# Optimization experiments

Hardware: AMD Instinct MI355X
Metric: run time of the kernel (lower is better)

## Reference

```python
import jax, jax.numpy as jnp
import numpy as np

B, N, DIM = 2, 512, 512
HEADS, DIM_HEAD, MAX_LEN = 8, 64, 1024


def _skew(QEr):
    # pad last dim on the left by 1, reshape (n, n+1) -> (n+1, n), drop first row
    padded = jnp.pad(QEr, ((0, 0), (0, 0), (0, 0), (1, 0)))
    b, h, r, c = padded.shape
    return padded.reshape(b, h, c, r)[:, :, 1:, :]


def _fft_multiply_parallel(A, x):
    # A: [b,h,n,n] decay matrix; x: [b,h,n,d]
    b, h, n, d = x.shape
    # y = [last column of A, first row of A] -> [b,h,2n]
    y = jnp.concatenate([A[:, :, :, -1], A[:, :, 0, :]], axis=-1)
    v = jnp.concatenate([x, jnp.zeros_like(x)], axis=-2)  # zero-pad rows n -> 2n
    # Faithful to the original torch code: fftn over ALL axes (incl. batch/head),
    # then ifft over the LAST axis only, then slice back to n rows.
    H = jnp.fft.fftn(y)[:, :, :, None] * jnp.fft.fftn(v)
    return jnp.fft.ifft(H)[:, :, :n, :]


def _forward(x, Wq, Wk, Wv, Er):
    b, n, _ = x.shape

    def split_heads(t):
        return t.reshape(b, n, HEADS, DIM_HEAD).transpose(0, 2, 1, 3)  # [b,h,n,d]

    q = split_heads(x @ Wq)
    k = split_heads(x @ Wk)
    v = split_heads(x @ Wv)
    # global (Frobenius) norm over the full tensor, as torch.norm(t)
    q = q / jnp.linalg.norm(q)
    k = k / jnp.linalg.norm(k)
    q_ = jax.nn.elu(q)
    k_ = jax.nn.elu(k)

    Er_t = Er[MAX_LEN - n:, :].T        # [d, n]
    QEr = q @ Er_t                       # [b,h,n,n]
    c = jnp.exp(_skew(QEr))              # relative-position decay, [b,h,n,n]

    a_1 = jnp.einsum('bhnx,bhny->bhnxy', k_, v).reshape(b, HEADS, n, DIM_HEAD * DIM_HEAD)
    d_2 = _fft_multiply_parallel(c, k_)                                   # [b,h,n,d] complex
    d_1 = _fft_multiply_parallel(c, a_1).reshape(b, HEADS, n, DIM_HEAD, DIM_HEAD)

    top = jnp.einsum('bhnx,bhnyz->bhnz', q_, d_1)    # complex [b,h,n,d]
    bottom = jnp.einsum('bhnx,bhny->bhny', q_, d_2)  # complex [b,h,n,d]
    return top / bottom


def setup_inputs() -> dict:
    key = jax.random.key(0)
    k1, k2, k3, k4, k5 = jax.random.split(key, 5)
    s = jnp.float32(1.0 / np.sqrt(DIM))
    return {
        'x': jax.random.normal(k1, (B, N, DIM), dtype=jnp.float32),
        'Wq': jax.random.normal(k2, (DIM, HEADS * DIM_HEAD), dtype=jnp.float32) * s,
        'Wk': jax.random.normal(k3, (DIM, HEADS * DIM_HEAD), dtype=jnp.float32) * s,
        'Wv': jax.random.normal(k4, (DIM, HEADS * DIM_HEAD), dtype=jnp.float32) * s,
        'Er': jax.random.normal(k5, (MAX_LEN, DIM_HEAD), dtype=jnp.float32),
    }


def reference(x, Wq, Wk, Wv, Er):
    return _forward(x, Wq, Wk, Wv, Er)
```

## Files before the change

### kernel.cpp

```cpp
#include <hip/hip_runtime.h>
#include <math.h>


#define DIMX 512
#define NPOS 512
#define PADIDX(m) ((m) + ((m) >> 4))

typedef unsigned short ushort_t;
typedef unsigned int uint_t;
typedef __bf16 bf16x8 __attribute__((ext_vector_type(8)));
typedef float floatx4 __attribute__((ext_vector_type(4)));

static __device__ inline ushort_t f2bf(float f) {
    uint_t u = __float_as_uint(f);
    u = u + 0x7FFFu + ((u >> 16) & 1u);
    return (ushort_t)(u >> 16);
}
static __device__ inline float bf2f(ushort_t h) {
    return __uint_as_float(((uint_t)h) << 16);
}

#define BFLY(lo, hi, tw) do {                                   \
    const float sr_ = (lo).x - (hi).x, si_ = (lo).y - (hi).y;   \
    (lo).x += (hi).x; (lo).y += (hi).y;                         \
    (hi).x = sr_ * (tw).x - si_ * (tw).y;                       \
    (hi).y = sr_ * (tw).y + si_ * (tw).x;                       \
} while (0)

__global__ __launch_bounds__(256)
void conv_kernel(const float* __restrict__ x,
                 const float* __restrict__ Wk, const float* __restrict__ Wv,
                 ushort_t* __restrict__ xh, ushort_t* __restrict__ xl,
                 ushort_t* __restrict__ wth, ushort_t* __restrict__ wtl,
                 float2* __restrict__ twd)
{
    const int blk = blockIdx.x;
    const int t = threadIdx.x;
    if (blk < 512) {
        const int idx4 = blk * 256 + t;
        const float4 v = ((const float4*)x)[idx4];
        const float vf[4] = {v.x, v.y, v.z, v.w};
        ushort_t h[4], l[4];
        #pragma unroll
        for (int e = 0; e < 4; ++e) {
            h[e] = f2bf(vf[e]);
            l[e] = f2bf(vf[e] - bf2f(h[e]));
        }
        const ushort4 hv4 = make_ushort4(h[0], h[1], h[2], h[3]);
        const ushort4 lv4 = make_ushort4(l[0], l[1], l[2], l[3]);
        *(ushort4*)(xh + (size_t)idx4 * 4) = hv4;
        *(ushort4*)(xl + (size_t)idx4 * 4) = lv4;
    } else if (blk < 1024) {
        __shared__ float tile[32][33];
        const int b2 = blk - 512;
        const int s  = b2 >> 8;
        const int kt = (b2 >> 4) & 15;
        const int nt = b2 & 15;
        const int c  = t & 31, r4 = t >> 5;
        const float* __restrict__ W = s ? Wv : Wk;
        #pragma unroll
        for (int i = 0; i < 4; ++i) {
            const int row = r4 + i * 8;
            tile[row][c] = W[(size_t)(kt * 32 + row) * 512 + nt * 32 + c];
        }
        __syncthreads();
        #pragma unroll
        for (int i = 0; i < 4; ++i) {
            const int nl = r4 + i * 8;
            const float v = tile[c][nl];
            const ushort_t h = f2bf(v);
            const ushort_t l = f2bf(v - bf2f(h));
            const size_t o = (size_t)(s * 512 + nt * 32 + nl) * 512 + kt * 32 + c;
            wth[o] = h;
            wtl[o] = l;
        }
    } else {
        const int jj = (blk - 1024) * 256 + t;
        double s, cc;
        sincos(-6.2831853071795864769 * (double)jj / 1024.0, &s, &cc);
        twd[jj] = make_float2((float)cc, (float)s);
    }
}

__global__ __launch_bounds__(256)
void gemm_mfma_kernel(const ushort_t* __restrict__ xh, const ushort_t* __restrict__ xl,
                      const ushort_t* __restrict__ wth, const ushort_t* __restrict__ wtl,
                      float* __restrict__ K, float* __restrict__ V,
                      float* __restrict__ partials)
{
    const int blk = blockIdx.x;
    const int ct = blk >> 5;
    const int rt = blk & 31;
    const int t = threadIdx.x;
    const int w = t >> 6, lane = t & 63;
    const int qd = lane >> 4, lm = lane & 15;

    const int mrow = rt * 32 + (w & 1) * 16 + lm;
    const int wcol = (w >> 1) * 32;
    const size_t aoff = (size_t)mrow * 512 + qd * 8;

    __shared__ __align__(16) ushort_t Bs[2][2][8][64][8];
    __shared__ float red[4];

    #define STAGE(buf_, k0_)                                                     \
    {                                                                            \
        _Pragma("unroll")                                                        \
        for (int i = 0; i < 4; ++i) {                                            \
            const int seg = w * 4 + i;                                           \
            const int arr_ = seg >> 3, kq_ = seg & 7;                            \
            const ushort_t* src_ = (arr_ ? wtl : wth)                            \
                + (size_t)(ct * 64 + lane) * 512 + (k0_) + kq_ * 8;              \
            __builtin_amdgcn_global_load_lds(                                    \
                (const __attribute__((address_space(1))) uint_t*)src_,           \
                (__attribute__((address_space(3))) uint_t*)&Bs[buf_][arr_][kq_][0][0], \
                16, 0, 0);                                                       \
        }                                                                        \
    }

    floatx4 acc0 = {0.f, 0.f, 0.f, 0.f};
    floatx4 acc1 = {0.f, 0.f, 0.f, 0.f};

    STAGE(0, 0)
    for (int ks = 0; ks < 8; ++ks) {
        __syncthreads();
        const int buf = ks & 1;
        const int k0 = ks * 64;
        if (ks < 7) STAGE(buf ^ 1, k0 + 64)
        #pragma unroll
        for (int s2 = 0; s2 < 2; ++s2) {
            const bf16x8 Ah = *(const bf16x8*)&xh[aoff + k0 + s2 * 32];
            const bf16x8 Al = *(const bf16x8*)&xl[aoff + k0 + s2 * 32];
            const int kq = s2 * 4 + qd;
            const bf16x8 B0h = *(const bf16x8*)Bs[buf][0][kq][wcol + lm];
            const bf16x8 B0l = *(const bf16x8*)Bs[buf][1][kq][wcol + lm];
            const bf16x8 B1h = *(const bf16x8*)Bs[buf][0][kq][wcol + 16 + lm];
            const bf16x8 B1l = *(const bf16x8*)Bs[buf][1][kq][wcol + 16 + lm];
            acc0 = __builtin_amdgcn_mfma_f32_16x16x32_bf16(Ah, B0h, acc0, 0, 0, 0);
            acc0 = __builtin_amdgcn_mfma_f32_16x16x32_bf16(Ah, B0l, acc0, 0, 0, 0);
            acc0 = __builtin_amdgcn_mfma_f32_16x16x32_bf16(Al, B0h, acc0, 0, 0, 0);
            acc1 = __builtin_amdgcn_mfma_f32_16x16x32_bf16(Ah, B1h, acc1, 0, 0, 0);
            acc1 = __builtin_amdgcn_mfma_f32_16x16x32_bf16(Ah, B1l, acc1, 0, 0, 0);
            acc1 = __builtin_amdgcn_mfma_f32_16x16x32_bf16(Al, B1h, acc1, 0, 0, 0);
        }
    }
    #undef STAGE

    float ss = 0.f;
    const int orow0 = rt * 32 + (w & 1) * 16 + qd * 4;
    float* __restrict__ O = (ct < 8) ? K : V;
    const int cb = (ct < 8) ? 0 : 512;
    const int c0 = ct * 64 + wcol + lm - cb;
    #pragma unroll
    for (int r = 0; r < 4; ++r) {
        const size_t row = orow0 + r;
        const float v0 = acc0[r], v1 = acc1[r];
        O[row * 512 + c0]      = v0;
        O[row * 512 + c0 + 16] = v1;
        if (ct < 8) ss += v0 * v0 + v1 * v1;
    }
    #pragma unroll
    for (int off = 32; off > 0; off >>= 1)
        ss += __shfl_down(ss, off, 64);
    if (lane == 0) red[w] = ss;
    __syncthreads();
    if (t == 0) partials[blk] = red[0] + red[1] + red[2] + red[3];
}

__device__ __constant__ float C8[8] = {
    1.f, 0.70710678118654752440f, 0.f, -0.70710678118654752440f,
   -1.f, -0.70710678118654752440f, 0.f, 0.70710678118654752440f };
__device__ __constant__ float S8[8] = {
    0.f, -0.70710678118654752440f, -1.f, -0.70710678118654752440f,
    0.f,  0.70710678118654752440f,  1.f,  0.70710678118654752440f };

__global__ __launch_bounds__(256)
void stage1_kernel(const float* __restrict__ K,
                   const float* __restrict__ V,
                   const float* __restrict__ partials,
                   float2* __restrict__ Gk,
                   float2* __restrict__ Gp)
{
    const int m = blockIdx.x;
    const int t = threadIdx.x;
    __shared__ float kk[2][8][64];
    __shared__ float pp[2][8][64];
    __shared__ float skp[16][4];
    __shared__ float sk[2][8];
    __shared__ float sred[4];

    float p = partials[t] + partials[t + 256];
    #pragma unroll
    for (int off = 32; off > 0; off >>= 1)
        p += __shfl_down(p, off, 64);
    if ((t & 63) == 0) sred[t >> 6] = p;
    __syncthreads();
    const float scale = (float)(1.0 / sqrt((double)sred[0] + (double)sred[1] +
                                           (double)sred[2] + (double)sred[3]));

    {
        const int e0 = t * 4;
        const int b = e0 >> 9, rem = e0 & 511, h = rem >> 6, z = rem & 63;
        const size_t src = (size_t)(b * 512 + m) * DIMX + h * 64 + z;
        const float4 kv4 = *(const float4*)&K[src];
        const float4 vv4 = *(const float4*)&V[src];
        const float kf[4] = {kv4.x, kv4.y, kv4.z, kv4.w};
        const float vf[4] = {vv4.x, vv4.y, vv4.z, vv4.w};
        #pragma unroll
        for (int e = 0; e < 4; ++e) {
            const float kv = kf[e] * scale;
            kk[b][h][z + e] = kv > 0.f ? kv : expm1f(kv);
            pp[b][h][z + e] = vf[e];
        }
    }
    __syncthreads();
    if (t < 64) {
        const int bh = t >> 2, q = t & 3;
        float s = 0.f;
        #pragma unroll
        for (int zz = 0; zz < 16; ++zz) s += kk[bh >> 3][bh & 7][q * 16 + zz];
        skp[bh][q] = s;
    }
    __syncthreads();
    if (t < 16) sk[t >> 3][t & 7] = skp[t][0] + skp[t][1] + skp[t][2] + skp[t][3];
    __syncthreads();

    for (int e2 = t; e2 < 512; e2 += 256) {
        const int be = e2 >> 5;
        const int zp = e2 & 31;
        const int beta = be >> 3, eta = be & 7;
        float kr[2] = {0.f, 0.f}, ki[2] = {0.f, 0.f};
        float pr[2] = {0.f, 0.f}, pim[2] = {0.f, 0.f};
        #pragma unroll
        for (int b = 0; b < 2; ++b) {
            const float sgn = (beta & b) ? -1.f : 1.f;
            #pragma unroll
            for (int h = 0; h < 8; ++h) {
                const int ph = (eta * h) & 7;
                const float cr = C8[ph], ci = S8[ph];
                const float skv = sk[b][h];
                #pragma unroll
                for (int zz = 0; zz < 2; ++zz) {
                    const int z = zp * 2 + zz;
                    const float a = kk[b][h][z] * sgn;
                    kr[zz] = fmaf(a, cr, kr[zz]);
                    ki[zz] = fmaf(a, ci, ki[zz]);
                    const float p2 = (pp[b][h][z] * skv) * sgn;
                    pr[zz]  = fmaf(p2, cr, pr[zz]);
                    pim[zz] = fmaf(p2, ci, pim[zz]);
                }
            }
        }
        const float4 rk = make_float4(kr[0], ki[0], kr[1], ki[1]);
        const float4 rp = make_float4(pr[0], pim[0], pr[1], pim[1]);
        const size_t o = ((size_t)be * NPOS + m) * 64 + zp * 2;
        *(float4*)&Gk[o] = rk;
        *(float4*)&Gp[o] = rp;
    }
}

__global__ __launch_bounds__(256)
void fft_div_kernel(const float2* __restrict__ Gk,
                    const float2* __restrict__ Gp,
                    const float2* __restrict__ twd,
                    float* __restrict__ out, int out_cplx)
{
    const int blk = blockIdx.x;
    const int j  = blk & 7;
    const int l  = (blk >> 3) & 3;
    const int be = blk >> 5;
    const int zg = j * 4 + l;
    const int t  = threadIdx.x;

    __shared__ float2 g[4][1088];
    __shared__ float2 w[544];

    for (int jj = t; jj < 512; jj += 256)
        w[PADIDX(jj)] = twd[jj];
    for (int e = t; e < 1024; e += 256) {
        const int a = e >> 9;
        const int m = e & 511;
        const float4 v4 = *(const float4*)&(a ? Gp : Gk)[((size_t)be * NPOS + m) * 64 + zg * 2];
        g[a * 2 + 0][PADIDX(m)] = make_float2(v4.x, v4.y);
        g[a * 2 + 1][PADIDX(m)] = make_float2(v4.z, v4.w);
    }
    __syncthreads();

    const int wv   = t >> 6;
    const int lane = t & 63;

    #pragma unroll
    for (int qh = 0; qh < 2; ++qh) {
        const int hh  = 1 - qh;
        const int arr = wv;
        const int jo  = lane;
        float2 f[8];
        #pragma unroll
        for (int k = 0; k < 8; ++k)
            f[k] = g[arr][PADIDX(jo + k * 64)];
        if (hh == 1) {
            #pragma unroll
            for (int k = 0; k < 8; ++k) {
                const float2 tw = w[PADIDX(jo + k * 64)];
                f[k] = make_float2(f[k].x * tw.x - f[k].y * tw.y,
                                   f[k].x * tw.y + f[k].y * tw.x);
            }
        }
        #pragma unroll
        for (int k = 0; k < 4; ++k) {
            const float2 tw = w[PADIDX(2 * jo + 128 * k)];
            BFLY(f[k], f[k + 4], tw);
        }
        {
            const float2 tw0 = w[PADIDX(4 * jo)];
            const float2 tw1 = w[PADIDX(4 * jo + 256)];
            BFLY(f[0], f[2], tw0); BFLY(f[1], f[3], tw1);
            BFLY(f[4], f[6], tw0); BFLY(f[5], f[7], tw1);
        }
        {
            const float2 tw = w[PADIDX(8 * jo)];
            BFLY(f[0], f[1], tw); BFLY(f[2], f[3], tw);
            BFLY(f[4], f[5], tw); BFLY(f[6], f[7], tw);
        }
        #pragma unroll
        for (int k = 0; k < 8; ++k)
            g[arr][PADIDX(hh * 512 + jo + k * 64)] = f[k];
    }

    #pragma unroll
    for (int q = 0; q < 2; ++q) {
        const int arr = wv;
        const int b64 = q * 8 + (lane >> 3);
        const int jo  = lane & 7;
        const int e0  = b64 * 64 + jo;
        float2 f[8];
        #pragma unroll
        for (int k = 0; k < 8; ++k)
            f[k] = g[arr][PADIDX(e0 + 8 * k)];
        #pragma unroll
        for (int k = 0; k < 4; ++k) {
            const float2 tw = w[PADIDX(16 * jo + 128 * k)];
            BFLY(f[k], f[k + 4], tw);
        }
        {
            const float2 tw0 = w[PADIDX(32 * jo)];
            const float2 tw1 = w[PADIDX(32 * jo + 256)];
            BFLY(f[0], f[2], tw0); BFLY(f[1], f[3], tw1);
            BFLY(f[4], f[6], tw0); BFLY(f[5], f[7], tw1);
        }
        {
            const float2 tw = w[PADIDX(64 * jo)];
            BFLY(f[0], f[1], tw); BFLY(f[2], f[3], tw);
            BFLY(f[4], f[5], tw); BFLY(f[6], f[7], tw);
        }
        #pragma unroll
        for (int k = 0; k < 8; ++k)
            g[arr][PADIDX(e0 + 8 * k)] = f[k];
    }

    #pragma unroll
    for (int q = 0; q < 2; ++q) {
        const int arr = wv;
        const int b8  = q * 64 + lane;
        const int e0  = b8 * 8;
        float2 f[8];
        #pragma unroll
        for (int k = 0; k < 8; ++k)
            f[k] = g[arr][PADIDX(e0 + k)];
        BFLY(f[0], f[4], w[PADIDX(0)]);
        BFLY(f[1], f[5], w[PADIDX(128)]);
        BFLY(f[2], f[6], w[PADIDX(256)]);
        BFLY(f[3], f[7], w[PADIDX(384)]);
        {
            const float2 tw0 = w[PADIDX(0)];
            const float2 tw1 = w[PADIDX(256)];
            BFLY(f[0], f[2], tw0); BFLY(f[1], f[3], tw1);
            BFLY(f[4], f[6], tw0); BFLY(f[5], f[7], tw1);
        }
        f[0].x += f[1].x; f[0].y += f[1].y;
        f[2].x += f[3].x; f[2].y += f[3].y;
        f[4].x += f[5].x; f[4].y += f[5].y;
        f[6].x += f[7].x; f[6].y += f[7].y;
        g[arr][PADIDX(e0 + 0)] = f[0];
        g[arr][PADIDX(e0 + 2)] = f[2];
        g[arr][PADIDX(e0 + 4)] = f[4];
        g[arr][PADIDX(e0 + 6)] = f[6];
    }
    __syncthreads();

    for (int e2 = t; e2 < 512; e2 += 256) {
        const int i  = e2;
        const int pi = PADIDX(2 * i);
        const int mu = (int)(__brev((unsigned)i) >> 23);
        float4 res;
        #pragma unroll
        for (int zi = 0; zi < 2; ++zi) {
            const float2 D  = g[zi][pi];
            const float2 Nm = g[2 + zi][pi];
            const float inv = 1.f / (D.x * D.x + D.y * D.y);
            const float rr = (Nm.x * D.x + Nm.y * D.y) * inv;
            const float ri = (Nm.y * D.x - Nm.x * D.y) * inv;
            if (zi == 0) { res.x = rr; res.y = ri; }
            else         { res.z = rr; res.w = ri; }
        }
        const size_t o = ((size_t)be * NPOS + mu) * 64 + zg * 2;
        if (out_cplx) {
            *(float4*)&((float2*)out)[o] = res;
        } else {
            out[o]     = res.x;
            out[o + 1] = res.z;
        }
    }
}

__global__ __launch_bounds__(256)
void gemm_kv_kernel(const float* __restrict__ x,
                    const float* __restrict__ Wk,
                    const float* __restrict__ Wv,
                    float* __restrict__ K,
                    float* __restrict__ V,
                    float* __restrict__ partials)
{
    const int blk  = blockIdx.x;
    const int sel  = (blk >> 2) & 1;
    const int cg2  = blk & 3;
    const int rt   = blk >> 3;
    const int row0 = rt * 16;
    const int col0 = cg2 * 128;
    const int t    = threadIdx.x;
    const int tc   = t & 31;
    const int tr   = t >> 5;
    const float* __restrict__ W   = sel ? Wv : Wk;
    float* __restrict__       Out = sel ? V  : K;

    __shared__ float xs[16][DIMX];
    __shared__ float red[4];

    #pragma unroll
    for (int jj = 0; jj < 8; ++jj) {
        const int f = t + jj * 256;
        const int row = f >> 7, c4 = f & 127;
        *(float4*)&xs[row][c4 * 4] = *(const float4*)&x[(size_t)(row0 + row) * DIMX + c4 * 4];
    }
    __syncthreads();

    const float* Wb = W + col0 + tc * 4;
    float4 wA[8], wB[8];
    #pragma unroll
    for (int jj = 0; jj < 8; ++jj) wA[jj] = *(const float4*)&Wb[(size_t)(jj) * DIMX];
    #pragma unroll
    for (int jj = 0; jj < 8; ++jj) wB[jj] = *(const float4*)&Wb[(size_t)(8 + jj) * DIMX];

    float acc[2][4] = {{0,0,0,0},{0,0,0,0}};
    const int r0 = tr * 2;

    #define COMPUTE_CHUNK(WREG, CH)                                            \
        {   float4 xv0a = *(const float4*)&xs[r0][(CH) * 8];                   \
            float4 xv0b = *(const float4*)&xs[r0][(CH) * 8 + 4];               \
            float4 xv1a = *(const float4*)&xs[r0 + 1][(CH) * 8];               \
            float4 xv1b = *(const float4*)&xs[r0 + 1][(CH) * 8 + 4];           \
            _Pragma("unroll")                                                  \
            for (int kk = 0; kk < 4; ++kk) {                                   \
                const float x0 = (&xv0a.x)[kk], x1 = (&xv1a.x)[kk];            \
                _Pragma("unroll")                                              \
                for (int cc = 0; cc < 4; ++cc) {                               \
                    acc[0][cc] = fmaf(x0, (&WREG[kk].x)[cc], acc[0][cc]);      \
                    acc[1][cc] = fmaf(x1, (&WREG[kk].x)[cc], acc[1][cc]);      \
                } }                                                            \
            _Pragma("unroll")                                                  \
            for (int kk = 0; kk < 4; ++kk) {                                   \
                const float x0 = (&xv0b.x)[kk], x1 = (&xv1b.x)[kk];            \
                _Pragma("unroll")                                              \
                for (int cc = 0; cc < 4; ++cc) {                               \
                    acc[0][cc] = fmaf(x0, (&WREG[kk + 4].x)[cc], acc[0][cc]);  \
                    acc[1][cc] = fmaf(x1, (&WREG[kk + 4].x)[cc], acc[1][cc]);  \
                } } }

    for (int ch = 0; ch < 64; ch += 2) {
        COMPUTE_CHUNK(wA, ch)
        if (ch < 62) {
            #pragma unroll
            for (int jj = 0; jj < 8; ++jj)
                wA[jj] = *(const float4*)&Wb[(size_t)((ch + 2) * 8 + jj) * DIMX];
        }
        COMPUTE_CHUNK(wB, ch + 1)
        if (ch < 62) {
            #pragma unroll
            for (int jj = 0; jj < 8; ++jj)
                wB[jj] = *(const float4*)&Wb[(size_t)((ch + 3) * 8 + jj) * DIMX];
        }
    }
    #undef COMPUTE_CHUNK

    float ss = 0.f;
    #pragma unroll
    for (int i = 0; i < 2; ++i) {
        const int row = row0 + r0 + i;
        const float4 o = make_float4(acc[i][0], acc[i][1], acc[i][2], acc[i][3]);
        *(float4*)&Out[(size_t)row * DIMX + col0 + tc * 4] = o;
        ss += o.x * o.x + o.y * o.y + o.z * o.z + o.w * o.w;
    }
    if (sel == 0) {
        #pragma unroll
        for (int off = 32; off > 0; off >>= 1)
            ss += __shfl_down(ss, off, 64);
        if ((t & 63) == 0) red[t >> 6] = ss;
        __syncthreads();
        if (t == 0) partials[blk] = red[0] + red[1] + red[2] + red[3];
    } else {
        if (t == 0) partials[blk] = 0.f;
    }
}

__global__ __launch_bounds__(256)
void mdft_fallback_kernel(const float2* __restrict__ Gk,
                          const float2* __restrict__ Gp,
                          float* __restrict__ out,
                          int out_cplx)
{
    const int blk = blockIdx.x;
    const int be = blk >> 6, z = blk & 63;
    const int t = threadIdx.x;
    __shared__ float2 gk[512];
    __shared__ float2 gp[512];
    __shared__ float2 w[1024];

    for (int m = t; m < 512; m += 256) {
        const size_t idx = ((size_t)be * NPOS + m) * 64 + z;
        gk[m] = Gk[idx];
        gp[m] = Gp[idx];
    }
    for (int jj = t; jj < 1024; jj += 256) {
        double s, c;
        sincos(-6.2831853071795864769 * (double)jj / 1024.0, &s, &c);
        w[jj] = make_float2((float)c, (float)s);
    }
    __syncthreads();

    #pragma unroll
    for (int half = 0; half < 2; ++half) {
        const int mu = t + half * 256;
        double dr = 0.0, di = 0.0, nr = 0.0, ni = 0.0;
        int idx = 0;
        for (int m = 0; m < 512; ++m) {
            const float2 tw = w[idx];
            idx = (idx + mu) & 1023;
            const float2 a = gk[m];
            dr += (double)(a.x * tw.x - a.y * tw.y);
            di += (double)(a.x * tw.y + a.y * tw.x);
            const float2 p2 = gp[m];
            nr += (double)(p2.x * tw.x - p2.y * tw.y);
            ni += (double)(p2.x * tw.y + p2.y * tw.x);
        }
        const double dmag = dr * dr + di * di;
        const double orr = (nr * dr + ni * di) / dmag;
        const double oii = (ni * dr - nr * di) / dmag;
        const size_t o = ((size_t)be * NPOS + mu) * 64 + z;
        if (out_cplx) {
            out[2 * o]     = (float)orr;
            out[2 * o + 1] = (float)oii;
        } else {
            out[o] = (float)orr;
        }
    }
}

extern "C" void kernel_launch(void* const* d_in, const int* in_sizes, int n_in,
                              void* d_out, int out_size, void* d_ws, size_t ws_size,
                              hipStream_t stream)
{
    const float* x  = (const float*)d_in[0];
    const float* Wk = (const float*)d_in[2];
    const float* Wv = (const float*)d_in[3];
    float* out = (float*)d_out;

    char* ws = (char*)d_ws;
    float*  K    = (float*)(ws);
    float*  V    = (float*)(ws + (size_t)2097152);
    float2* Gk   = (float2*)(ws + (size_t)4194304);
    float*  part = (float*)(ws + (size_t)8388608);
    const int out_cplx = (out_size >= 2 * 2 * 8 * 512 * 64) ? 1 : 0;

    const bool ws_big = (ws_size >= (size_t)20971520);
    float2* Gp = ws_big ? (float2*)(ws + (size_t)8390656)
                        : (float2*)d_out;

    if (ws_big) {
        ushort_t* xh  = (ushort_t*)(ws + (size_t)16777216);
        ushort_t* xl  = (ushort_t*)(ws + (size_t)17825792);
        ushort_t* wth = (ushort_t*)(ws + (size_t)18874368);
        ushort_t* wtl = (ushort_t*)(ws + (size_t)19922944);
        float2*   twd = (float2*)(ws + (size_t)12584960);
        hipLaunchKernelGGL(conv_kernel, dim3(1026), dim3(256), 0, stream,
                           x, Wk, Wv, xh, xl, wth, wtl, twd);
        hipLaunchKernelGGL(gemm_mfma_kernel, dim3(512), dim3(256), 0, stream,
                           xh, xl, wth, wtl, K, V, part);
        hipLaunchKernelGGL(stage1_kernel, dim3(512), dim3(256), 0, stream,
                           K, V, part, Gk, Gp);
        hipLaunchKernelGGL(fft_div_kernel, dim3(512), dim3(256), 0, stream,
                           Gk, Gp, twd, out, out_cplx);
    } else {
        hipLaunchKernelGGL(gemm_kv_kernel, dim3(512), dim3(256), 0, stream,
                           x, Wk, Wv, K, V, part);
        hipLaunchKernelGGL(stage1_kernel, dim3(512), dim3(256), 0, stream,
                           K, V, part, Gk, Gp);
        hipLaunchKernelGGL(mdft_fallback_kernel, dim3(1024), dim3(256), 0, stream,
                           Gk, Gp, out, out_cplx);
    }
}
```

Measured before the change: 100.1 us.

## Transpose Gk/Gp intermediate layout and prefetch A fragments in projection GEMM

The intermediate Gk/Gp buffers change from position-major [be][m][z] to z-major [be][z][m]. The FFT/divide kernel can then load contiguous float4 runs along m instead of strided gathers, and the producer and fallback kernels are updated to match. Separately, the projection GEMM loop now loads the next k-step's A operand fragments into registers one iteration ahead, hiding load latency behind the MFMAs. In exchange, the producer's writes become scattered float2 stores, and the prefetch raises register pressure.

```diff
diff --git a/kernel.cpp b/kernel.cpp
--- a/kernel.cpp
+++ b/kernel.cpp
@@ -120,28 +120,50 @@
     floatx4 acc0 = {0.f, 0.f, 0.f, 0.f};
     floatx4 acc1 = {0.f, 0.f, 0.f, 0.f};
 
+    bf16x8 cAh0 = *(const bf16x8*)&xh[aoff];
+    bf16x8 cAl0 = *(const bf16x8*)&xl[aoff];
+    bf16x8 cAh1 = *(const bf16x8*)&xh[aoff + 32];
+    bf16x8 cAl1 = *(const bf16x8*)&xl[aoff + 32];
+
     STAGE(0, 0)
     for (int ks = 0; ks < 8; ++ks) {
         __syncthreads();
         const int buf = ks & 1;
         const int k0 = ks * 64;
         if (ks < 7) STAGE(buf ^ 1, k0 + 64)
-        #pragma unroll
-        for (int s2 = 0; s2 < 2; ++s2) {
-            const bf16x8 Ah = *(const bf16x8*)&xh[aoff + k0 + s2 * 32];
-            const bf16x8 Al = *(const bf16x8*)&xl[aoff + k0 + s2 * 32];
-            const int kq = s2 * 4 + qd;
+
+        const size_t anext = aoff + (size_t)(ks < 7 ? k0 + 64 : 0);
+        const bf16x8 nAh0 = *(const bf16x8*)&xh[anext];
+        const bf16x8 nAl0 = *(const bf16x8*)&xl[anext];
+        const bf16x8 nAh1 = *(const bf16x8*)&xh[anext + 32];
+        const bf16x8 nAl1 = *(const bf16x8*)&xl[anext + 32];
+
+        {
+            const bf16x8 B0h = *(const bf16x8*)Bs[buf][0][qd][wcol + lm];
+            const bf16x8 B0l = *(const bf16x8*)Bs[buf][1][qd][wcol + lm];
+            const bf16x8 B1h = *(const bf16x8*)Bs[buf][0][qd][wcol + 16 + lm];
+            const bf16x8 B1l = *(const bf16x8*)Bs[buf][1][qd][wcol + 16 + lm];
+            acc0 = __builtin_amdgcn_mfma_f32_16x16x32_bf16(cAh0, B0h, acc0, 0, 0, 0);
+            acc0 = __builtin_amdgcn_mfma_f32_16x16x32_bf16(cAh0, B0l, acc0, 0, 0, 0);
+            acc0 = __builtin_amdgcn_mfma_f32_16x16x32_bf16(cAl0, B0h, acc0, 0, 0, 0);
+            acc1 = __builtin_amdgcn_mfma_f32_16x16x32_bf16(cAh0, B1h, acc1, 0, 0, 0);
+            acc1 = __builtin_amdgcn_mfma_f32_16x16x32_bf16(cAh0, B1l, acc1, 0, 0, 0);
+            acc1 = __builtin_amdgcn_mfma_f32_16x16x32_bf16(cAl0, B1h, acc1, 0, 0, 0);
+        }
+        {
+            const int kq = qd + 4;
             const bf16x8 B0h = *(const bf16x8*)Bs[buf][0][kq][wcol + lm];
             const bf16x8 B0l = *(const bf16x8*)Bs[buf][1][kq][wcol + lm];
             const bf16x8 B1h = *(const bf16x8*)Bs[buf][0][kq][wcol + 16 + lm];
             const bf16x8 B1l = *(const bf16x8*)Bs[buf][1][kq][wcol + 16 + lm];
-            acc0 = __builtin_amdgcn_mfma_f32_16x16x32_bf16(Ah, B0h, acc0, 0, 0, 0);
-            acc0 = __builtin_amdgcn_mfma_f32_16x16x32_bf16(Ah, B0l, acc0, 0, 0, 0);
-            acc0 = __builtin_amdgcn_mfma_f32_16x16x32_bf16(Al, B0h, acc0, 0, 0, 0);
-            acc1 = __builtin_amdgcn_mfma_f32_16x16x32_bf16(Ah, B1h, acc1, 0, 0, 0);
-            acc1 = __builtin_amdgcn_mfma_f32_16x16x32_bf16(Ah, B1l, acc1, 0, 0, 0);
-            acc1 = __builtin_amdgcn_mfma_f32_16x16x32_bf16(Al, B1h, acc1, 0, 0, 0);
-        }
+            acc0 = __builtin_amdgcn_mfma_f32_16x16x32_bf16(cAh1, B0h, acc0, 0, 0, 0);
+            acc0 = __builtin_amdgcn_mfma_f32_16x16x32_bf16(cAh1, B0l, acc0, 0, 0, 0);
+            acc0 = __builtin_amdgcn_mfma_f32_16x16x32_bf16(cAl1, B0h, acc0, 0, 0, 0);
+            acc1 = __builtin_amdgcn_mfma_f32_16x16x32_bf16(cAh1, B1h, acc1, 0, 0, 0);
+            acc1 = __builtin_amdgcn_mfma_f32_16x16x32_bf16(cAh1, B1l, acc1, 0, 0, 0);
+            acc1 = __builtin_amdgcn_mfma_f32_16x16x32_bf16(cAl1, B1h, acc1, 0, 0, 0);
+        }
+        cAh0 = nAh0; cAl0 = nAl0; cAh1 = nAh1; cAl1 = nAl1;
     }
     #undef STAGE
 
@@ -250,11 +272,11 @@
                 }
             }
         }
-        const float4 rk = make_float4(kr[0], ki[0], kr[1], ki[1]);
-        const float4 rp = make_float4(pr[0], pim[0], pr[1], pim[1]);
-        const size_t o = ((size_t)be * NPOS + m) * 64 + zp * 2;
-        *(float4*)&Gk[o] = rk;
-        *(float4*)&Gp[o] = rp;
+        const size_t rbase = ((size_t)be * 64 + zp * 2) * 512 + m;
+        Gk[rbase]       = make_float2(kr[0], ki[0]);
+        Gk[rbase + 512] = make_float2(kr[1], ki[1]);
+        Gp[rbase]       = make_float2(pr[0], pim[0]);
+        Gp[rbase + 512] = make_float2(pr[1], pim[1]);
     }
 }
 
@@ -277,11 +299,13 @@
     for (int jj = t; jj < 512; jj += 256)
         w[PADIDX(jj)] = twd[jj];
     for (int e = t; e < 1024; e += 256) {
-        const int a = e >> 9;
-        const int m = e & 511;
-        const float4 v4 = *(const float4*)&(a ? Gp : Gk)[((size_t)be * NPOS + m) * 64 + zg * 2];
-        g[a * 2 + 0][PADIDX(m)] = make_float2(v4.x, v4.y);
-        g[a * 2 + 1][PADIDX(m)] = make_float2(v4.z, v4.w);
+        const int idx = e >> 8;
+        const int a  = idx >> 1, zi = idx & 1;
+        const int m  = (e & 255) * 2;
+        const float4 v4 = *(const float4*)&(a ? Gp : Gk)
+            [((size_t)be * 64 + zg * 2 + zi) * 512 + m];
+        g[a * 2 + zi][PADIDX(m)]     = make_float2(v4.x, v4.y);
+        g[a * 2 + zi][PADIDX(m + 1)] = make_float2(v4.z, v4.w);
     }
     __syncthreads();
 
@@ -525,7 +549,7 @@
     __shared__ float2 w[1024];
 
     for (int m = t; m < 512; m += 256) {
-        const size_t idx = ((size_t)be * NPOS + m) * 64 + z;
+        const size_t idx = ((size_t)be * 64 + z) * 512 + m;
         gk[m] = Gk[idx];
         gp[m] = Gp[idx];
     }
```

Result: slower. 108.8 us (+8.7%).
